# Performance work log

Hardware: AMD Instinct MI355X
Metric: run time of the kernel (lower is better)

## Reference

```python
import jax, jax.numpy as jnp
import numpy as np

N, E, F_IN, HID, HEADS, NCLS = 50000, 800000, 500, 16, 8, 40
NEG_SLOPE = 0.2


def setup_inputs() -> dict:
    key = jax.random.key(0)
    ks = jax.random.split(key, 10)
    x = jax.random.normal(ks[0], (N, F_IN), jnp.float32)
    edge_index = jax.random.randint(ks[1], (2, E), 0, N)
    W1 = jax.random.normal(ks[2], (F_IN, HEADS * HID), jnp.float32) * (1.0 / np.sqrt(F_IN))
    a_src1 = jax.random.normal(ks[3], (HEADS, HID), jnp.float32) * 0.1
    a_dst1 = jax.random.normal(ks[4], (HEADS, HID), jnp.float32) * 0.1
    b1 = jnp.zeros((HEADS * HID,), jnp.float32)
    W2 = jax.random.normal(ks[5], (HEADS * HID, NCLS), jnp.float32) * (1.0 / np.sqrt(HEADS * HID))
    a_src2 = jax.random.normal(ks[6], (1, NCLS), jnp.float32) * 0.1
    a_dst2 = jax.random.normal(ks[7], (1, NCLS), jnp.float32) * 0.1
    b2 = jnp.zeros((NCLS,), jnp.float32)
    return {"x": x, "edge_index": edge_index, "W1": W1, "a_src1": a_src1,
            "a_dst1": a_dst1, "b1": b1, "W2": W2, "a_src2": a_src2,
            "a_dst2": a_dst2, "b2": b2}


def gat_layer(x, edge_index, W, a_src, a_dst, b, heads, ch, concat):
    n = x.shape[0]
    h = (x @ W).reshape(n, heads, ch)                 # [N,H,C]
    alpha_src = jnp.sum(h * a_src, axis=-1)           # [N,H]
    alpha_dst = jnp.sum(h * a_dst, axis=-1)           # [N,H]
    loop = jnp.arange(n)                              # PyG add_self_loops=True
    src = jnp.concatenate([edge_index[0], loop])
    dst = jnp.concatenate([edge_index[1], loop])
    e = jax.nn.leaky_relu(alpha_src[src] + alpha_dst[dst], NEG_SLOPE)  # [E',H]
    # segment softmax over destination nodes
    m = jax.ops.segment_max(e, dst, num_segments=n)
    ex = jnp.exp(e - m[dst])
    denom = jax.ops.segment_sum(ex, dst, num_segments=n)
    alpha = ex / (denom[dst] + 1e-16)                 # [E',H]
    out = jax.ops.segment_sum(h[src] * alpha[:, :, None], dst, num_segments=n)  # [N,H,C]
    out = out.reshape(n, heads * ch) if concat else out.mean(axis=1)
    return out + b


def reference(x, edge_index, W1, a_src1, a_dst1, b1, W2, a_src2, a_dst2, b2):
    h = jax.nn.elu(gat_layer(x, edge_index, W1, a_src1, a_dst1, b1, HEADS, HID, True))
    # dropout p=0.6 is identity in eval mode
    h = gat_layer(h, edge_index, W2, a_src2, a_dst2, b2, 1, NCLS, False)
    return jax.nn.log_softmax(h, axis=1)
```

## Files before the change

kernel.cpp:

```cpp
#include <hip/hip_runtime.h>
#include <hip/hip_bf16.h>
#include <math.h>

#define N_NODES 50000
#define F_IN    500
#define HEADS   8
#define HID     16
#define HH      128
#define NCLS    40
#define NEG     0.2f

typedef _Float16 f16x2 __attribute__((ext_vector_type(2)));
typedef _Float16 f16x4 __attribute__((ext_vector_type(4)));
typedef _Float16 f16x8 __attribute__((ext_vector_type(8)));
typedef float    f32x4 __attribute__((ext_vector_type(4)));

__device__ __forceinline__ float lrelu(float x) { return x >= 0.f ? x : NEG * x; }

__global__ void convW_kernel(const float* __restrict__ W1, _Float16* __restrict__ Wt) {
    int i = blockIdx.x * 256 + threadIdx.x;
    if (i >= 128 * 512) return;
    int c = i >> 9, k = i & 511;
    Wt[i] = (k < F_IN) ? (_Float16)W1[k * HH + c] : (_Float16)0.f;
}

#define KT   128
#define LDP  136
__global__ __launch_bounds__(256) void gemm1_mfma(const float* __restrict__ x,
                                                  const _Float16* __restrict__ Wt,
                                                  _Float16* __restrict__ h1h) {
    __shared__ _Float16 As[64 * LDP];
    __shared__ _Float16 Bs[128 * LDP];
    const int t = threadIdx.x;
    const int lane = t & 63, w = t >> 6;
    const int rowBase = blockIdx.x * 64;

    f32x4 acc[8];
#pragma unroll
    for (int n = 0; n < 8; ++n) acc[n] = (f32x4){0.f, 0.f, 0.f, 0.f};

    const int fa = t & 31, ra = t >> 5;
    const int gb = t & 15, cb = t >> 4;

    for (int kt = 0; kt < 4; ++kt) {
        const int kt0 = kt * KT;
#pragma unroll
        for (int p = 0; p < 8; ++p) {
            int row = ra + 8 * p;
            int grow = rowBase + row;
            int k0 = kt0 + 4 * fa;
            float4 v = make_float4(0.f, 0.f, 0.f, 0.f);
            if (grow < N_NODES && k0 < F_IN)
                v = *(const float4*)&x[(size_t)grow * F_IN + k0];
            f16x4 hv = {(_Float16)v.x, (_Float16)v.y, (_Float16)v.z, (_Float16)v.w};
            *(f16x4*)&As[row * LDP + 4 * fa] = hv;
        }
#pragma unroll
        for (int p = 0; p < 8; ++p) {
            int c = cb + 16 * p;
            *(f16x8*)&Bs[c * LDP + 8 * gb] = *(const f16x8*)&Wt[c * 512 + kt0 + 8 * gb];
        }
        __syncthreads();
#pragma unroll
        for (int ks = 0; ks < 4; ++ks) {
            int kk = ks * 32 + (lane >> 4) * 8;
            f16x8 a = *(const f16x8*)&As[(16 * w + (lane & 15)) * LDP + kk];
#pragma unroll
            for (int n = 0; n < 8; ++n) {
                f16x8 b = *(const f16x8*)&Bs[(16 * n + (lane & 15)) * LDP + kk];
                acc[n] = __builtin_amdgcn_mfma_f32_16x16x32_f16(a, b, acc[n], 0, 0, 0);
            }
        }
        __syncthreads();
    }
    const int colb = lane & 15, rq = lane >> 4;
#pragma unroll
    for (int n = 0; n < 8; ++n) {
#pragma unroll
        for (int r = 0; r < 4; ++r) {
            int grow = rowBase + 16 * w + rq * 4 + r;
            if (grow < N_NODES) h1h[(size_t)grow * HH + 16 * n + colb] = (_Float16)acc[n][r];
        }
    }
}

__global__ void alpha1_kernel(const _Float16* __restrict__ h1h,
                              const float* __restrict__ a_src,
                              const float* __restrict__ a_dst,
                              float* __restrict__ asrc, float* __restrict__ adst) {
    int idx = blockIdx.x * blockDim.x + threadIdx.x;
    if (idx >= N_NODES * HEADS) return;
    int n = idx >> 3, h = idx & 7;
    const f16x8* hp = (const f16x8*)&h1h[(size_t)n * HH + h * HID];
    float s = 0.f, d = 0.f;
#pragma unroll
    for (int c = 0; c < 2; ++c) {
        f16x8 hv = hp[c];
#pragma unroll
        for (int i = 0; i < 8; ++i) {
            float f = (float)hv[i];
            s += f * a_src[h * HID + c * 8 + i];
            d += f * a_dst[h * HID + c * 8 + i];
        }
    }
    asrc[idx] = s;
    adst[idx] = d;
}

__global__ void zero_int_kernel(int* __restrict__ p, int n) {
    int i = blockIdx.x * blockDim.x + threadIdx.x;
    if (i < n) p[i] = 0;
}

__global__ void count_kernel(const int* __restrict__ ei, int* __restrict__ deg,
                             int E, int EP) {
    int e = blockIdx.x * blockDim.x + threadIdx.x;
    if (e >= EP) return;
    int dst = (e < E) ? ei[E + e] : (e - E);
    atomicAdd(&deg[dst], 1);
}

__global__ __launch_bounds__(1024) void scan_kernel(const int* __restrict__ deg,
                                                    int* __restrict__ offs,
                                                    int* __restrict__ cursor, int n) {
    __shared__ int part[1024];
    int tid = threadIdx.x;
    int chunk = (n + 1023) / 1024;
    int start = tid * chunk;
    int end = min(start + chunk, n);
    int s = 0;
    for (int i = start; i < end; i++) s += deg[i];
    part[tid] = s;
    __syncthreads();
    for (int off = 1; off < 1024; off <<= 1) {
        int v = 0;
        if (tid >= off) v = part[tid - off];
        __syncthreads();
        if (tid >= off) part[tid] += v;
        __syncthreads();
    }
    int base = (tid == 0) ? 0 : part[tid - 1];
    for (int i = start; i < end; i++) {
        offs[i] = base;
        cursor[i] = base;
        base += deg[i];
    }
    if (tid == 1023) offs[n] = base;
}

__global__ void fill_kernel(const int* __restrict__ ei, int* __restrict__ cursor,
                            int* __restrict__ bsrc, int E, int EP) {
    int e = blockIdx.x * blockDim.x + threadIdx.x;
    if (e >= EP) return;
    int src, dst;
    if (e < E) { src = ei[e]; dst = ei[E + e]; }
    else       { src = e - E; dst = e - E; }
    int slot = atomicAdd(&cursor[dst], 1);
    bsrc[slot] = src;
}

__global__ __launch_bounds__(256) void agg1_kernel(const _Float16* __restrict__ h1h,
                                                   const float* __restrict__ asrc,
                                                   const float* __restrict__ adst,
                                                   const int* __restrict__ offs,
                                                   const int* __restrict__ bsrc,
                                                   const float* __restrict__ b1,
                                                   _Float16* __restrict__ h1bh) {
    int lane = threadIdx.x & 63;
    int node = blockIdx.x * 4 + (threadIdx.x >> 6);
    if (node >= N_NODES) return;
    int beg = offs[node], end = offs[node + 1];
    int hh = lane >> 3;
    float adv = adst[node * 8 + hh];

    float acc0 = 0.f, acc1 = 0.f, dsum = 0.f;
    int j = beg;
    for (; j + 2 <= end; j += 2) {
        int s0 = bsrc[j], s1 = bsrc[j + 1];
        float sa0 = asrc[s0 * 8 + hh];
        float sa1 = asrc[s1 * 8 + hh];
        f16x2 hv0 = *(const f16x2*)&h1h[(size_t)s0 * HH + 2 * lane];
        f16x2 hv1 = *(const f16x2*)&h1h[(size_t)s1 * HH + 2 * lane];
        float w0 = __expf(lrelu(sa0 + adv));
        float w1 = __expf(lrelu(sa1 + adv));
        dsum += w0 + w1;
        acc0 += w0 * (float)hv0[0] + w1 * (float)hv1[0];
        acc1 += w0 * (float)hv0[1] + w1 * (float)hv1[1];
    }
    if (j < end) {
        int s0 = bsrc[j];
        float sa0 = asrc[s0 * 8 + hh];
        f16x2 hv0 = *(const f16x2*)&h1h[(size_t)s0 * HH + 2 * lane];
        float w0 = __expf(lrelu(sa0 + adv));
        dsum += w0;
        acc0 += w0 * (float)hv0[0];
        acc1 += w0 * (float)hv0[1];
    }
    float rv = 1.f / (dsum + 1e-16f);
    float2 bv = *(const float2*)&b1[2 * lane];
    float v0 = acc0 * rv + bv.x;
    float v1 = acc1 * rv + bv.y;
    v0 = v0 > 0.f ? v0 : __expf(v0) - 1.f;
    v1 = v1 > 0.f ? v1 : __expf(v1) - 1.f;
    f16x2 o = {(_Float16)v0, (_Float16)v1};
    *(f16x2*)&h1bh[(size_t)node * HH + 2 * lane] = o;
}

__global__ __launch_bounds__(256) void gemm2_kernel(const _Float16* __restrict__ h1bh,
                                                    const float* __restrict__ W2,
                                                    _Float16* __restrict__ h2h) {
    __shared__ float Ws[HH * NCLS];
    for (int i = threadIdx.x; i < HH * NCLS; i += 256) Ws[i] = W2[i];
    __syncthreads();
    int idx = blockIdx.x * 256 + threadIdx.x;
    if (idx >= N_NODES * NCLS) return;
    int n = idx / NCLS, c = idx - n * NCLS;
    const f16x8* hp = (const f16x8*)&h1bh[(size_t)n * HH];
    float acc = 0.f;
#pragma unroll
    for (int k8 = 0; k8 < HH / 8; ++k8) {
        f16x8 hv = hp[k8];
#pragma unroll
        for (int i = 0; i < 8; ++i)
            acc += (float)hv[i] * Ws[(k8 * 8 + i) * NCLS + c];
    }
    h2h[idx] = (_Float16)acc;
}

__global__ void alpha2_kernel(const _Float16* __restrict__ h2h,
                              const float* __restrict__ a_src,
                              const float* __restrict__ a_dst,
                              float* __restrict__ asrc, float* __restrict__ adst) {
    int n = blockIdx.x * blockDim.x + threadIdx.x;
    if (n >= N_NODES) return;
    const f16x8* hp = (const f16x8*)&h2h[(size_t)n * NCLS];
    float s = 0.f, d = 0.f;
#pragma unroll
    for (int c8 = 0; c8 < NCLS / 8; ++c8) {
        f16x8 hv = hp[c8];
#pragma unroll
        for (int i = 0; i < 8; ++i) {
            float f = (float)hv[i];
            s += f * a_src[c8 * 8 + i];
            d += f * a_dst[c8 * 8 + i];
        }
    }
    asrc[n] = s;
    adst[n] = d;
}

__global__ __launch_bounds__(256) void agg2_kernel(const _Float16* __restrict__ h2h,
                                                   const float* __restrict__ asrc,
                                                   const float* __restrict__ adst,
                                                   const int* __restrict__ offs,
                                                   const int* __restrict__ bsrc,
                                                   const float* __restrict__ b2,
                                                   float* __restrict__ out) {
    int lane = threadIdx.x & 63;
    int node = blockIdx.x * 4 + (threadIdx.x >> 6);
    if (node >= N_NODES) return;
    int beg = offs[node], end = offs[node + 1];
    float adv = adst[node];
    bool act = lane < NCLS / 2;

    float acc0 = 0.f, acc1 = 0.f, dsum = 0.f;
    int j = beg;
    for (; j + 2 <= end; j += 2) {
        int s0 = bsrc[j], s1 = bsrc[j + 1];
        float w0 = __expf(lrelu(asrc[s0] + adv));
        float w1 = __expf(lrelu(asrc[s1] + adv));
        f16x2 hv0 = {(_Float16)0.f, (_Float16)0.f}, hv1 = hv0;
        if (act) {
            hv0 = *(const f16x2*)&h2h[(size_t)s0 * NCLS + 2 * lane];
            hv1 = *(const f16x2*)&h2h[(size_t)s1 * NCLS + 2 * lane];
        }
        dsum += w0 + w1;
        acc0 += w0 * (float)hv0[0] + w1 * (float)hv1[0];
        acc1 += w0 * (float)hv0[1] + w1 * (float)hv1[1];
    }
    if (j < end) {
        int s0 = bsrc[j];
        float w0 = __expf(lrelu(asrc[s0] + adv));
        f16x2 hv0 = {(_Float16)0.f, (_Float16)0.f};
        if (act) hv0 = *(const f16x2*)&h2h[(size_t)s0 * NCLS + 2 * lane];
        dsum += w0;
        acc0 += w0 * (float)hv0[0];
        acc1 += w0 * (float)hv0[1];
    }
    float rd = 1.f / (dsum + 1e-16f);
    float v0 = -1e30f, v1 = -1e30f;
    if (act) {
        float2 bv = *(const float2*)&b2[2 * lane];
        v0 = acc0 * rd + bv.x;
        v1 = acc1 * rd + bv.y;
    }
    float m = fmaxf(v0, v1);
#pragma unroll
    for (int o = 32; o; o >>= 1) m = fmaxf(m, __shfl_xor(m, o, 64));
    float p = act ? (__expf(v0 - m) + __expf(v1 - m)) : 0.f;
#pragma unroll
    for (int o = 32; o; o >>= 1) p += __shfl_xor(p, o, 64);
    float ls = m + __logf(p);
    if (act) {
        float2 ov = make_float2(v0 - ls, v1 - ls);
        *(float2*)&out[(size_t)node * NCLS + 2 * lane] = ov;
    }
}

extern "C" void kernel_launch(void* const* d_in, const int* in_sizes, int n_in,
                              void* d_out, int out_size, void* d_ws, size_t ws_size,
                              hipStream_t stream) {
    const float* x      = (const float*)d_in[0];
    const int*   ei     = (const int*)d_in[1];
    const float* W1     = (const float*)d_in[2];
    const float* a_src1 = (const float*)d_in[3];
    const float* a_dst1 = (const float*)d_in[4];
    const float* b1     = (const float*)d_in[5];
    const float* W2     = (const float*)d_in[6];
    const float* a_src2 = (const float*)d_in[7];
    const float* a_dst2 = (const float*)d_in[8];
    const float* b2     = (const float*)d_in[9];
    float* out = (float*)d_out;

    const int E  = in_sizes[1] / 2;
    const int EP = E + N_NODES;

    char* w = (char*)d_ws;
    _Float16* h1h   = (_Float16*)(w + 0);
    _Float16* h1bh  = (_Float16*)(w + 12800000);
    float*    asrc1 = (float*)(w + 25600000);
    float*    adst1 = (float*)(w + 27200000);
    _Float16* h2h   = (_Float16*)(w + 28800000);
    float*    asrc2 = (float*)(w + 32800000);
    float*    adst2 = (float*)(w + 33000000);
    int*      deg   = (int*)(w + 33200000);
    int*      offs  = (int*)(w + 33400064);
    int*      cursor= (int*)(w + 33600128);
    int*      bsrc  = (int*)(w + 33800192);
    _Float16* Wt    = (_Float16*)(w + 37200256);

    zero_int_kernel<<<(N_NODES + 255) / 256, 256, 0, stream>>>(deg, N_NODES);
    convW_kernel<<<(128 * 512 + 255) / 256, 256, 0, stream>>>(W1, Wt);
    gemm1_mfma<<<(N_NODES + 63) / 64, 256, 0, stream>>>(x, Wt, h1h);
    alpha1_kernel<<<(N_NODES * HEADS + 255) / 256, 256, 0, stream>>>(h1h, a_src1, a_dst1,
                                                                     asrc1, adst1);
    count_kernel<<<(EP + 255) / 256, 256, 0, stream>>>(ei, deg, E, EP);
    scan_kernel<<<1, 1024, 0, stream>>>(deg, offs, cursor, N_NODES);
    fill_kernel<<<(EP + 255) / 256, 256, 0, stream>>>(ei, cursor, bsrc, E, EP);
    agg1_kernel<<<(N_NODES + 3) / 4, 256, 0, stream>>>(h1h, asrc1, adst1, offs, bsrc, b1, h1bh);
    gemm2_kernel<<<(N_NODES * NCLS + 255) / 256, 256, 0, stream>>>(h1bh, W2, h2h);
    alpha2_kernel<<<(N_NODES + 255) / 256, 256, 0, stream>>>(h2h, a_src2, a_dst2,
                                                             asrc2, adst2);
    agg2_kernel<<<(N_NODES + 3) / 4, 256, 0, stream>>>(h2h, asrc2, adst2, offs, bsrc, b2, out);
}
```

Measured before the change: 547.9 us.

## Replace single-block prefix scan with three-pass multi-block scan

The degree prefix sum previously ran in one 1024-thread block, with each thread serially scanning about 49 uncoalesced elements. It now uses a per-block scan, a single-block scan of the 196 block sums, and a pass that adds the block offsets, so the work spreads across many CUs with coalesced accesses. The cost is two extra kernel launches. The block-sum step assumes there are at most 256 blocks, which holds for 50000 nodes.

```diff
diff --git a/kernel.cpp b/kernel.cpp
--- a/kernel.cpp
+++ b/kernel.cpp
@@ -120,32 +120,52 @@
     atomicAdd(&deg[dst], 1);
 }
 
-__global__ __launch_bounds__(1024) void scan_kernel(const int* __restrict__ deg,
+__global__ __launch_bounds__(256) void scan1_kernel(const int* __restrict__ deg,
                                                     int* __restrict__ offs,
-                                                    int* __restrict__ cursor, int n) {
-    __shared__ int part[1024];
+                                                    int* __restrict__ bsums, int n) {
+    __shared__ int sm[256];
+    int tid = threadIdx.x, i = blockIdx.x * 256 + tid;
+    int v = (i < n) ? deg[i] : 0;
+    sm[tid] = v;
+    __syncthreads();
+    for (int off = 1; off < 256; off <<= 1) {
+        int t = 0;
+        if (tid >= off) t = sm[tid - off];
+        __syncthreads();
+        if (tid >= off) sm[tid] += t;
+        __syncthreads();
+    }
+    if (i < n) offs[i] = sm[tid] - v;
+    if (tid == 255) bsums[blockIdx.x] = sm[255];
+}
+
+__global__ __launch_bounds__(256) void scan2_kernel(const int* __restrict__ bsums,
+                                                    int* __restrict__ boffs, int nb,
+                                                    int* __restrict__ offs, int n) {
+    __shared__ int sm[256];
     int tid = threadIdx.x;
-    int chunk = (n + 1023) / 1024;
-    int start = tid * chunk;
-    int end = min(start + chunk, n);
-    int s = 0;
-    for (int i = start; i < end; i++) s += deg[i];
-    part[tid] = s;
+    int v = (tid < nb) ? bsums[tid] : 0;
+    sm[tid] = v;
     __syncthreads();
-    for (int off = 1; off < 1024; off <<= 1) {
-        int v = 0;
-        if (tid >= off) v = part[tid - off];
-        __syncthreads();
-        if (tid >= off) part[tid] += v;
-        __syncthreads();
-    }
-    int base = (tid == 0) ? 0 : part[tid - 1];
-    for (int i = start; i < end; i++) {
-        offs[i] = base;
-        cursor[i] = base;
-        base += deg[i];
-    }
-    if (tid == 1023) offs[n] = base;
+    for (int off = 1; off < 256; off <<= 1) {
+        int t = 0;
+        if (tid >= off) t = sm[tid - off];
+        __syncthreads();
+        if (tid >= off) sm[tid] += t;
+        __syncthreads();
+    }
+    if (tid < nb) boffs[tid] = sm[tid] - v;
+    if (tid == 255) offs[n] = sm[255];
+}
+
+__global__ __launch_bounds__(256) void scan3_kernel(int* __restrict__ offs,
+                                                    int* __restrict__ cursor,
+                                                    const int* __restrict__ boffs, int n) {
+    int i = blockIdx.x * 256 + threadIdx.x;
+    if (i >= n) return;
+    int o = offs[i] + boffs[blockIdx.x];
+    offs[i] = o;
+    cursor[i] = o;
 }
 
 __global__ void fill_kernel(const int* __restrict__ ei, int* __restrict__ cursor,
@@ -324,6 +344,7 @@
 
     const int E  = in_sizes[1] / 2;
     const int EP = E + N_NODES;
+    const int NB = (N_NODES + 255) / 256;
 
     char* w = (char*)d_ws;
     _Float16* h1h   = (_Float16*)(w + 0);
@@ -338,6 +359,8 @@
     int*      cursor= (int*)(w + 33600128);
     int*      bsrc  = (int*)(w + 33800192);
     _Float16* Wt    = (_Float16*)(w + 37200256);
+    int*      bsums = (int*)(w + 37331328);
+    int*      boffs = (int*)(w + 37332352);
 
     zero_int_kernel<<<(N_NODES + 255) / 256, 256, 0, stream>>>(deg, N_NODES);
     convW_kernel<<<(128 * 512 + 255) / 256, 256, 0, stream>>>(W1, Wt);
@@ -345,7 +368,9 @@
     alpha1_kernel<<<(N_NODES * HEADS + 255) / 256, 256, 0, stream>>>(h1h, a_src1, a_dst1,
                                                                      asrc1, adst1);
     count_kernel<<<(EP + 255) / 256, 256, 0, stream>>>(ei, deg, E, EP);
-    scan_kernel<<<1, 1024, 0, stream>>>(deg, offs, cursor, N_NODES);
+    scan1_kernel<<<NB, 256, 0, stream>>>(deg, offs, bsums, N_NODES);
+    scan2_kernel<<<1, 256, 0, stream>>>(bsums, boffs, NB, offs, N_NODES);
+    scan3_kernel<<<NB, 256, 0, stream>>>(offs, cursor, boffs, N_NODES);
     fill_kernel<<<(EP + 255) / 256, 256, 0, stream>>>(ei, cursor, bsrc, E, EP);
     agg1_kernel<<<(N_NODES + 3) / 4, 256, 0, stream>>>(h1h, asrc1, adst1, offs, bsrc, b1, h1bh);
     gemm2_kernel<<<(N_NODES * NCLS + 255) / 256, 256, 0, stream>>>(h1bh, W2, h2h);
```

Measured after the change: 446.7 us. -18.5%, faster.
